# Kernel optimization log

Hardware: AMD Instinct MI355X
Metric: run time of the kernel (lower is better)

The kernel has to match this reference:

```python
import jax, jax.numpy as jnp
import numpy as np

B, N, M = 1, 16384, 16384
K_NEIGH = 16
KERNEL_SIZE = 15
C_IN, C_OUT = 64, 128
RADIUS = 1.0


def setup_inputs() -> dict:
    key = jax.random.key(0)
    k1, k2, k3, k4, k5 = jax.random.split(key, 5)
    query_points = jax.random.normal(k1, (B, N, 3), dtype=jnp.float32)
    support_points = query_points  # typical KPConv: support == query
    neighbor_idx = jax.random.randint(k2, (B, N, K_NEIGH), 0, M)
    features = jax.random.normal(k3, (B, M, C_IN), dtype=jnp.float32)
    weights = jax.random.normal(k4, (KERNEL_SIZE, C_IN, C_OUT), dtype=jnp.float32) * 0.005
    # kernel points: random unit directions scaled to radius, first fixed at center
    kp = jax.random.normal(k5, (KERNEL_SIZE, 3), dtype=jnp.float32)
    kp = kp / jnp.linalg.norm(kp, axis=1, keepdims=True) * RADIUS
    kernel_points = kp.at[0].set(jnp.zeros(3, dtype=jnp.float32))
    return {
        "query_points": query_points,
        "support_points": support_points,
        "neighbor_idx": neighbor_idx,
        "features": features,
        "weights": weights,
        "kernel_points": kernel_points,
    }


def reference(query_points, support_points, neighbor_idx, features, weights, kernel_points):
    # gather neighbor features and coords: (B,N,k,C), (B,N,k,3)
    gather = jax.vmap(lambda arr, idx: arr[idx])
    neighbor_feats = gather(features, neighbor_idx)
    neighbor_coords = gather(support_points, neighbor_idx)
    # relative coords to query: (B,N,k,3)
    rel = neighbor_coords - query_points[:, :, None, :]
    # distance to each kernel point: (B,N,k,P)
    diff = rel[:, :, :, None, :] - kernel_points[None, None, None, :, :]
    dists = jnp.linalg.norm(diff, axis=-1)
    # linear influence
    infl = jnp.clip(1.0 - dists / RADIUS, 0.0)
    # weighted sum over neighbors -> (B,N,P,C) without materializing (B,N,k,P,C)
    aggregated = jnp.einsum('bnkp,bnkc->bnpc', infl, neighbor_feats)
    # per-kernel-point matmul -> (B,N,C_out)
    return jnp.einsum('bnpc,pco->bno', aggregated, weights)
```

## Files before the change

kernel.cpp:

```cpp
#include <hip/hip_runtime.h>

typedef __attribute__((ext_vector_type(8))) short bf16x8;
typedef __attribute__((ext_vector_type(4))) float f32x4;

constexpr int N_PTS = 16384;
constexpr int KN = 16;
constexpr int P  = 15;
constexpr int CI = 64;
constexpr int CO = 128;
constexpr int QB = 16;
constexpr int KTOT   = P * CI;
constexpr int KSTEPS = KTOT / 32;
constexpr int NTILES = CO / 16;
constexpr int AGG_PITCH = KTOT + 8;

static __device__ __forceinline__ unsigned short f2bf(float f) {
    unsigned u = __float_as_uint(f);
    u = (u + 0x7fffu + ((u >> 16) & 1u)) >> 16;
    return (unsigned short)u;
}

__global__ __launch_bounds__(256) void prep_w(const float* __restrict__ W,
                                              unsigned short* __restrict__ WB) {
    const int t = blockIdx.x * 256 + threadIdx.x;
    const int s  = t >> 9;
    const int nt = (t >> 6) & 7;
    const int l  = t & 63;
    const int kb = s * 32 + ((l >> 4) * 8);
    const int o  = nt * 16 + (l & 15);
    unsigned short v[8];
    #pragma unroll
    for (int j = 0; j < 8; ++j) {
        v[j] = f2bf(W[(size_t)(kb + j) * CO + o]);
    }
    uint4 q;
    q.x = v[0] | ((unsigned)v[1] << 16);
    q.y = v[2] | ((unsigned)v[3] << 16);
    q.z = v[4] | ((unsigned)v[5] << 16);
    q.w = v[6] | ((unsigned)v[7] << 16);
    *(uint4*)&WB[(size_t)t * 8] = q;
}

__global__ __launch_bounds__(256) void kpconv_main(
    const float* __restrict__ query,
    const float* __restrict__ support,
    const int*   __restrict__ nidx,
    const float* __restrict__ feats,
    const unsigned short* __restrict__ WB,
    const float* __restrict__ kp,
    float* __restrict__ out)
{
    __shared__ float sKp[P][3];
    __shared__ int   sIdx[QB][KN];
    __shared__ __align__(16) float sInfl[QB][KN][16];
    __shared__ __align__(16) unsigned short sAgg[QB][AGG_PITCH];

    const int t  = threadIdx.x;
    const int n0 = blockIdx.x * QB;

    if (t < P * 3) ((float*)sKp)[t] = kp[t];
    __syncthreads();

    {
        const int pt = t >> 4, k = t & 15;
        const int n = n0 + pt;
        const int idx = nidx[n * KN + k];
        sIdx[pt][k] = idx;
        const float rx = support[idx * 3 + 0] - query[n * 3 + 0];
        const float ry = support[idx * 3 + 1] - query[n * 3 + 1];
        const float rz = support[idx * 3 + 2] - query[n * 3 + 2];
        #pragma unroll
        for (int p = 0; p < P; ++p) {
            const float dx = rx - sKp[p][0];
            const float dy = ry - sKp[p][1];
            const float dz = rz - sKp[p][2];
            sInfl[pt][k][p] = fmaxf(1.0f - sqrtf(dx*dx + dy*dy + dz*dz), 0.0f);
        }
        sInfl[pt][k][15] = 0.0f;
    }
    __syncthreads();

    {
        const int pt = t >> 4;
        const int c  = (t & 15) * 4;
        int idxv[KN];
        {
            const int4* ip = (const int4*)sIdx[pt];
            #pragma unroll
            for (int k4 = 0; k4 < 4; ++k4) {
                const int4 v = ip[k4];
                idxv[k4*4+0] = v.x; idxv[k4*4+1] = v.y;
                idxv[k4*4+2] = v.z; idxv[k4*4+3] = v.w;
            }
        }
        float acc[P][4];
        #pragma unroll
        for (int p = 0; p < P; ++p)
            #pragma unroll
            for (int j = 0; j < 4; ++j) acc[p][j] = 0.0f;

        #pragma unroll
        for (int k = 0; k < KN; ++k) {
            const float4 f = *(const float4*)&feats[(size_t)idxv[k] * CI + c];
            float iv[16];
            {
                const float4* ip = (const float4*)sInfl[pt][k];
                *(float4*)&iv[0]  = ip[0];
                *(float4*)&iv[4]  = ip[1];
                *(float4*)&iv[8]  = ip[2];
                *(float4*)&iv[12] = ip[3];
            }
            #pragma unroll
            for (int p = 0; p < P; ++p) {
                acc[p][0] = fmaf(iv[p], f.x, acc[p][0]);
                acc[p][1] = fmaf(iv[p], f.y, acc[p][1]);
                acc[p][2] = fmaf(iv[p], f.z, acc[p][2]);
                acc[p][3] = fmaf(iv[p], f.w, acc[p][3]);
            }
        }
        #pragma unroll
        for (int p = 0; p < P; ++p) {
            uint2 w;
            w.x = f2bf(acc[p][0]) | ((unsigned)f2bf(acc[p][1]) << 16);
            w.y = f2bf(acc[p][2]) | ((unsigned)f2bf(acc[p][3]) << 16);
            *(uint2*)&sAgg[pt][p * CI + c] = w;
        }
    }
    __syncthreads();

    {
        const int w = t >> 6, l = t & 63;
        const int row = l & 15;
        const int kq  = (l >> 4) * 8;
        f32x4 c0 = {0.f, 0.f, 0.f, 0.f};
        f32x4 c1 = {0.f, 0.f, 0.f, 0.f};
        const unsigned short* aggRow = &sAgg[row][kq];
        const unsigned short* wb0 = &WB[(size_t)((0 * NTILES + 2 * w) * 64 + l) * 8];
        #pragma unroll 2
        for (int s = 0; s < KSTEPS; ++s) {
            const bf16x8 a  = *(const bf16x8*)&aggRow[s * 32];
            const bf16x8 b0 = *(const bf16x8*)&wb0[(size_t)(s * NTILES) * 64 * 8];
            const bf16x8 b1 = *(const bf16x8*)&wb0[(size_t)(s * NTILES + 1) * 64 * 8];
            c0 = __builtin_amdgcn_mfma_f32_16x16x32_bf16(a, b0, c0, 0, 0, 0);
            c1 = __builtin_amdgcn_mfma_f32_16x16x32_bf16(a, b1, c1, 0, 0, 0);
        }
        const int rbase = (l >> 4) * 4;
        const int o0 = (2 * w) * 16 + (l & 15);
        #pragma unroll
        for (int r = 0; r < 4; ++r) {
            const int pt = rbase + r;
            out[(size_t)(n0 + pt) * CO + o0]      = c0[r];
            out[(size_t)(n0 + pt) * CO + o0 + 16] = c1[r];
        }
    }
}

extern "C" void kernel_launch(void* const* d_in, const int* in_sizes, int n_in,
                              void* d_out, int out_size, void* d_ws, size_t ws_size,
                              hipStream_t stream) {
    const float* query   = (const float*)d_in[0];
    const float* support = (const float*)d_in[1];
    const int*   nidx    = (const int*)d_in[2];
    const float* feats   = (const float*)d_in[3];
    const float* W       = (const float*)d_in[4];
    const float* kp      = (const float*)d_in[5];
    float* out = (float*)d_out;
    unsigned short* WB = (unsigned short*)d_ws;

    hipLaunchKernelGGL(prep_w, dim3(KSTEPS * NTILES * 64 / 256), dim3(256), 0, stream, W, WB);
    hipLaunchKernelGGL(kpconv_main, dim3(N_PTS / QB), dim3(256), 0, stream,
                       query, support, nidx, feats, WB, kp, out);
}
```

Baseline: 97.10 us.

## Split aggregation and GEMM into separate kernels with LDS-staged MFMA GEMM

```diff
diff --git a/kernel.cpp b/kernel.cpp
--- a/kernel.cpp
+++ b/kernel.cpp
@@ -12,7 +12,7 @@
 constexpr int KTOT   = P * CI;
 constexpr int KSTEPS = KTOT / 32;
 constexpr int NTILES = CO / 16;
-constexpr int AGG_PITCH = KTOT + 8;
+constexpr size_t AGG_BYTE_OFF = 262144;
 
 static __device__ __forceinline__ unsigned short f2bf(float f) {
     unsigned u = __float_as_uint(f);
@@ -20,40 +20,43 @@
     return (unsigned short)u;
 }
 
-__global__ __launch_bounds__(256) void prep_w(const float* __restrict__ W,
-                                              unsigned short* __restrict__ WB) {
-    const int t = blockIdx.x * 256 + threadIdx.x;
-    const int s  = t >> 9;
-    const int nt = (t >> 6) & 7;
-    const int l  = t & 63;
-    const int kb = s * 32 + ((l >> 4) * 8);
-    const int o  = nt * 16 + (l & 15);
-    unsigned short v[8];
-    #pragma unroll
-    for (int j = 0; j < 8; ++j) {
-        v[j] = f2bf(W[(size_t)(kb + j) * CO + o]);
-    }
-    uint4 q;
-    q.x = v[0] | ((unsigned)v[1] << 16);
-    q.y = v[2] | ((unsigned)v[3] << 16);
-    q.z = v[4] | ((unsigned)v[5] << 16);
-    q.w = v[6] | ((unsigned)v[7] << 16);
-    *(uint4*)&WB[(size_t)t * 8] = q;
-}
-
-__global__ __launch_bounds__(256) void kpconv_main(
+static __device__ __forceinline__ void gload16(const void* g, void* l) {
+    __builtin_amdgcn_global_load_lds(
+        (const __attribute__((address_space(1))) unsigned*)g,
+        (__attribute__((address_space(3))) unsigned*)l, 16, 0, 0);
+}
+
+__global__ __launch_bounds__(256) void kpconv_agg(
     const float* __restrict__ query,
     const float* __restrict__ support,
     const int*   __restrict__ nidx,
     const float* __restrict__ feats,
-    const unsigned short* __restrict__ WB,
+    const float* __restrict__ W,
     const float* __restrict__ kp,
-    float* __restrict__ out)
+    unsigned short* __restrict__ WB,
+    unsigned short* __restrict__ aggG)
 {
+    if (blockIdx.x < 60) {
+        const int t = blockIdx.x * 256 + threadIdx.x;
+        const int s  = t >> 9;
+        const int nt = (t >> 6) & 7;
+        const int l  = t & 63;
+        const int kb = s * 32 + ((l >> 4) * 8);
+        const int o  = nt * 16 + (l & 15);
+        unsigned short v[8];
+        #pragma unroll
+        for (int j = 0; j < 8; ++j) v[j] = f2bf(W[(size_t)(kb + j) * CO + o]);
+        uint4 q;
+        q.x = v[0] | ((unsigned)v[1] << 16);
+        q.y = v[2] | ((unsigned)v[3] << 16);
+        q.z = v[4] | ((unsigned)v[5] << 16);
+        q.w = v[6] | ((unsigned)v[7] << 16);
+        *(uint4*)&WB[(size_t)t * 8] = q;
+    }
+
     __shared__ float sKp[P][3];
     __shared__ int   sIdx[QB][KN];
     __shared__ __align__(16) float sInfl[QB][KN][16];
-    __shared__ __align__(16) unsigned short sAgg[QB][AGG_PITCH];
 
     const int t  = threadIdx.x;
     const int n0 = blockIdx.x * QB;
@@ -118,39 +121,72 @@
                 acc[p][3] = fmaf(iv[p], f.w, acc[p][3]);
             }
         }
+        const size_t rowBase = (size_t)(n0 + pt) * KTOT;
         #pragma unroll
         for (int p = 0; p < P; ++p) {
             uint2 w;
             w.x = f2bf(acc[p][0]) | ((unsigned)f2bf(acc[p][1]) << 16);
             w.y = f2bf(acc[p][2]) | ((unsigned)f2bf(acc[p][3]) << 16);
-            *(uint2*)&sAgg[pt][p * CI + c] = w;
-        }
-    }
-    __syncthreads();
-
-    {
-        const int w = t >> 6, l = t & 63;
-        const int row = l & 15;
-        const int kq  = (l >> 4) * 8;
-        f32x4 c0 = {0.f, 0.f, 0.f, 0.f};
-        f32x4 c1 = {0.f, 0.f, 0.f, 0.f};
-        const unsigned short* aggRow = &sAgg[row][kq];
-        const unsigned short* wb0 = &WB[(size_t)((0 * NTILES + 2 * w) * 64 + l) * 8];
-        #pragma unroll 2
-        for (int s = 0; s < KSTEPS; ++s) {
-            const bf16x8 a  = *(const bf16x8*)&aggRow[s * 32];
-            const bf16x8 b0 = *(const bf16x8*)&wb0[(size_t)(s * NTILES) * 64 * 8];
-            const bf16x8 b1 = *(const bf16x8*)&wb0[(size_t)(s * NTILES + 1) * 64 * 8];
-            c0 = __builtin_amdgcn_mfma_f32_16x16x32_bf16(a, b0, c0, 0, 0, 0);
-            c1 = __builtin_amdgcn_mfma_f32_16x16x32_bf16(a, b1, c1, 0, 0, 0);
-        }
-        const int rbase = (l >> 4) * 4;
-        const int o0 = (2 * w) * 16 + (l & 15);
-        #pragma unroll
-        for (int r = 0; r < 4; ++r) {
-            const int pt = rbase + r;
-            out[(size_t)(n0 + pt) * CO + o0]      = c0[r];
-            out[(size_t)(n0 + pt) * CO + o0 + 16] = c1[r];
+            *(uint2*)&aggG[rowBase + p * CI + c] = w;
+        }
+    }
+}
+
+__global__ __launch_bounds__(512) void kpconv_gemm(
+    const unsigned short* __restrict__ aggG,
+    const unsigned short* __restrict__ WB,
+    float* __restrict__ out)
+{
+    __shared__ __align__(16) unsigned short sA[2][4 * 64 * 8];
+    __shared__ __align__(16) unsigned short sB[2][8 * 64 * 8];
+
+    const int t = threadIdx.x;
+    const int w = t >> 6, l = t & 63;
+    const int n0 = blockIdx.x * 64;
+
+    const int rt = w & 3;
+    const int ng = w >> 2;
+    const int q  = l >> 4;
+
+    f32x4 acc[4] = {{0.f,0.f,0.f,0.f},{0.f,0.f,0.f,0.f},
+                    {0.f,0.f,0.f,0.f},{0.f,0.f,0.f,0.f}};
+
+    #define STAGE(s, b)                                                        \
+        do {                                                                   \
+            if (w < 4) {                                                       \
+                gload16(&aggG[(size_t)(n0 + l) * KTOT + (s) * 32 + w * 8],     \
+                        &sA[b][w * 512]);                                      \
+            } else {                                                           \
+                const int j = w - 4;                                           \
+                gload16(&WB[((size_t)(s) * 512 + j * 64 + l) * 8],             \
+                        &sB[b][j * 512]);                                      \
+                gload16(&WB[((size_t)(s) * 512 + (j + 4) * 64 + l) * 8],       \
+                        &sB[b][(j + 4) * 512]);                                \
+            }                                                                  \
+        } while (0)
+
+    STAGE(0, 0);
+    int b = 0;
+    for (int s = 0; s < KSTEPS; ++s) {
+        __syncthreads();
+        if (s + 1 < KSTEPS) STAGE(s + 1, b ^ 1);
+        const bf16x8 a = *(const bf16x8*)&sA[b][q * 512 + (rt * 16 + (l & 15)) * 8];
+        #pragma unroll
+        for (int nt = 0; nt < 4; ++nt) {
+            const bf16x8 bb = *(const bf16x8*)&sB[b][(ng * 4 + nt) * 512 + l * 8];
+            acc[nt] = __builtin_amdgcn_mfma_f32_16x16x32_bf16(a, bb, acc[nt], 0, 0, 0);
+        }
+        b ^= 1;
+    }
+    #undef STAGE
+
+    const int colBase = ng * 64;
+    const int rowBase = n0 + rt * 16 + (l >> 4) * 4;
+    #pragma unroll
+    for (int nt = 0; nt < 4; ++nt) {
+        #pragma unroll
+        for (int j = 0; j < 4; ++j) {
+            out[(size_t)(rowBase + j) * CO + colBase + nt * 16 + (l & 15)] = acc[nt][j];
         }
     }
 }
@@ -165,9 +201,12 @@
     const float* W       = (const float*)d_in[4];
     const float* kp      = (const float*)d_in[5];
     float* out = (float*)d_out;
-    unsigned short* WB = (unsigned short*)d_ws;
-
-    hipLaunchKernelGGL(prep_w, dim3(KSTEPS * NTILES * 64 / 256), dim3(256), 0, stream, W, WB);
-    hipLaunchKernelGGL(kpconv_main, dim3(N_PTS / QB), dim3(256), 0, stream,
-                       query, support, nidx, feats, WB, kp, out);
-}
+
+    unsigned short* WB   = (unsigned short*)d_ws;
+    unsigned short* aggG = (unsigned short*)((char*)d_ws + AGG_BYTE_OFF);
+
+    hipLaunchKernelGGL(kpconv_agg, dim3(N_PTS / QB), dim3(256), 0, stream,
+                       query, support, nidx, feats, W, kp, WB, aggG);
+    hipLaunchKernelGGL(kpconv_gemm, dim3(N_PTS / 64), dim3(512), 0, stream,
+                       aggG, WB, out);
+}
```

Result: slower. 105.2 us (+8.4%).

## Compute neighbor aggregation with MFMA and permute weights to match layout

Applied to the files above, without the earlier changes.

```diff
diff --git a/kernel.cpp b/kernel.cpp
--- a/kernel.cpp
+++ b/kernel.cpp
@@ -9,15 +9,21 @@
 constexpr int CI = 64;
 constexpr int CO = 128;
 constexpr int QB = 16;
-constexpr int KTOT   = P * CI;
-constexpr int KSTEPS = KTOT / 32;
-constexpr int NTILES = CO / 16;
-constexpr int AGG_PITCH = KTOT + 8;
+constexpr int KP = 1024;
+constexpr int KSTEPS = KP / 32;
+constexpr int IPITCH = 32;
+constexpr int APITCH = KP + 8;
 
 static __device__ __forceinline__ unsigned short f2bf(float f) {
     unsigned u = __float_as_uint(f);
     u = (u + 0x7fffu + ((u >> 16) & 1u)) >> 16;
     return (unsigned short)u;
+}
+
+static __device__ __forceinline__ unsigned cvt_pk_bf16(float lo, float hi) {
+    unsigned r;
+    asm("v_cvt_pk_bf16_f32 %0, %1, %2" : "=v"(r) : "v"(lo), "v"(hi));
+    return r;
 }
 
 __global__ __launch_bounds__(256) void prep_w(const float* __restrict__ W,
@@ -26,22 +32,28 @@
     const int s  = t >> 9;
     const int nt = (t >> 6) & 7;
     const int l  = t & 63;
-    const int kb = s * 32 + ((l >> 4) * 8);
+    const int q  = l >> 4;
     const int o  = nt * 16 + (l & 15);
     unsigned short v[8];
     #pragma unroll
     for (int j = 0; j < 8; ++j) {
-        v[j] = f2bf(W[(size_t)(kb + j) * CO + o]);
+        const int kp_ = s * 32 + q * 8 + j;
+        const int prodlane = kp_ >> 4;
+        const int ct = (kp_ >> 2) & 3;
+        const int jr = kp_ & 3;
+        const int p  = (prodlane >> 4) * 4 + jr;
+        const int c  = (prodlane & 15) + ct * 16;
+        v[j] = (p < P) ? f2bf(W[(size_t)(p * CI + c) * CO + o]) : (unsigned short)0;
     }
-    uint4 q;
-    q.x = v[0] | ((unsigned)v[1] << 16);
-    q.y = v[2] | ((unsigned)v[3] << 16);
-    q.z = v[4] | ((unsigned)v[5] << 16);
-    q.w = v[6] | ((unsigned)v[7] << 16);
-    *(uint4*)&WB[(size_t)t * 8] = q;
+    uint4 qv;
+    qv.x = v[0] | ((unsigned)v[1] << 16);
+    qv.y = v[2] | ((unsigned)v[3] << 16);
+    qv.z = v[4] | ((unsigned)v[5] << 16);
+    qv.w = v[6] | ((unsigned)v[7] << 16);
+    *(uint4*)&WB[(size_t)t * 8] = qv;
 }
 
-__global__ __launch_bounds__(256) void kpconv_main(
+__global__ __launch_bounds__(256) void kpconv_fused(
     const float* __restrict__ query,
     const float* __restrict__ support,
     const int*   __restrict__ nidx,
@@ -52,13 +64,20 @@
 {
     __shared__ float sKp[P][3];
     __shared__ int   sIdx[QB][KN];
-    __shared__ __align__(16) float sInfl[QB][KN][16];
-    __shared__ __align__(16) unsigned short sAgg[QB][AGG_PITCH];
+    __shared__ __align__(16) unsigned short sInflT[QB * 16 * IPITCH];
+    __shared__ __align__(16) unsigned short sAgg[QB * APITCH];
 
     const int t  = threadIdx.x;
     const int n0 = blockIdx.x * QB;
+    const int l  = t & 63, w = t >> 6, q = l >> 4;
 
     if (t < P * 3) ((float*)sKp)[t] = kp[t];
+
+    {
+        const uint4 z = {0u, 0u, 0u, 0u};
+        uint4* dst = (uint4*)sInflT;
+        dst[t] = z; dst[t + 256] = z; dst[t + 512] = z; dst[t + 768] = z;
+    }
     __syncthreads();
 
     {
@@ -69,83 +88,73 @@
         const float rx = support[idx * 3 + 0] - query[n * 3 + 0];
         const float ry = support[idx * 3 + 1] - query[n * 3 + 1];
         const float rz = support[idx * 3 + 2] - query[n * 3 + 2];
+        unsigned short* row0 = &sInflT[(pt * 16) * IPITCH + k];
         #pragma unroll
         for (int p = 0; p < P; ++p) {
             const float dx = rx - sKp[p][0];
             const float dy = ry - sKp[p][1];
             const float dz = rz - sKp[p][2];
-            sInfl[pt][k][p] = fmaxf(1.0f - sqrtf(dx*dx + dy*dy + dz*dz), 0.0f);
-        }
-        sInfl[pt][k][15] = 0.0f;
-    }
-    __syncthreads();
-
-    {
-        const int pt = t >> 4;
-        const int c  = (t & 15) * 4;
-        int idxv[KN];
-        {
-            const int4* ip = (const int4*)sIdx[pt];
-            #pragma unroll
-            for (int k4 = 0; k4 < 4; ++k4) {
-                const int4 v = ip[k4];
-                idxv[k4*4+0] = v.x; idxv[k4*4+1] = v.y;
-                idxv[k4*4+2] = v.z; idxv[k4*4+3] = v.w;
-            }
-        }
-        float acc[P][4];
-        #pragma unroll
-        for (int p = 0; p < P; ++p)
-            #pragma unroll
-            for (int j = 0; j < 4; ++j) acc[p][j] = 0.0f;
-
-        #pragma unroll
-        for (int k = 0; k < KN; ++k) {
-            const float4 f = *(const float4*)&feats[(size_t)idxv[k] * CI + c];
-            float iv[16];
-            {
-                const float4* ip = (const float4*)sInfl[pt][k];
-                *(float4*)&iv[0]  = ip[0];
-                *(float4*)&iv[4]  = ip[1];
-                *(float4*)&iv[8]  = ip[2];
-                *(float4*)&iv[12] = ip[3];
-            }
-            #pragma unroll
-            for (int p = 0; p < P; ++p) {
-                acc[p][0] = fmaf(iv[p], f.x, acc[p][0]);
-                acc[p][1] = fmaf(iv[p], f.y, acc[p][1]);
-                acc[p][2] = fmaf(iv[p], f.z, acc[p][2]);
-                acc[p][3] = fmaf(iv[p], f.w, acc[p][3]);
-            }
-        }
-        #pragma unroll
-        for (int p = 0; p < P; ++p) {
-            uint2 w;
-            w.x = f2bf(acc[p][0]) | ((unsigned)f2bf(acc[p][1]) << 16);
-            w.y = f2bf(acc[p][2]) | ((unsigned)f2bf(acc[p][3]) << 16);
-            *(uint2*)&sAgg[pt][p * CI + c] = w;
+            const float infl = fmaxf(1.0f - sqrtf(dx*dx + dy*dy + dz*dz), 0.0f);
+            row0[p * IPITCH] = f2bf(infl);
         }
     }
     __syncthreads();
 
     {
-        const int w = t >> 6, l = t & 63;
-        const int row = l & 15;
-        const int kq  = (l >> 4) * 8;
+        const f32x4 zero4 = {0.f, 0.f, 0.f, 0.f};
+        for (int i = 0; i < 4; ++i) {
+            const int pt = w * 4 + i;
+            const bf16x8 a = *(const bf16x8*)&sInflT[(pt * 16 + (l & 15)) * IPITCH + q * 8];
+            float fv[4][8];
+            #pragma unroll
+            for (int j = 0; j < 8; ++j) {
+                const int idx = sIdx[pt][(q & 1) * 8 + j];
+                const float* rowp = feats + (size_t)idx * CI + (l & 15);
+                #pragma unroll
+                for (int ct = 0; ct < 4; ++ct) fv[ct][j] = rowp[ct * 16];
+            }
+            f32x4 aggv[4];
+            #pragma unroll
+            for (int ct = 0; ct < 4; ++ct) {
+                unsigned b0 = cvt_pk_bf16(fv[ct][0], fv[ct][1]);
+                unsigned b1 = cvt_pk_bf16(fv[ct][2], fv[ct][3]);
+                unsigned b2 = cvt_pk_bf16(fv[ct][4], fv[ct][5]);
+                unsigned b3 = cvt_pk_bf16(fv[ct][6], fv[ct][7]);
+                if (l >= 32) { b0 = 0; b1 = 0; b2 = 0; b3 = 0; }
+                union { unsigned u[4]; bf16x8 v; } bu;
+                bu.u[0] = b0; bu.u[1] = b1; bu.u[2] = b2; bu.u[3] = b3;
+                aggv[ct] = __builtin_amdgcn_mfma_f32_16x16x32_bf16(a, bu.v, zero4, 0, 0, 0);
+            }
+            uint4 w0, w1;
+            w0.x = cvt_pk_bf16(aggv[0][0], aggv[0][1]);
+            w0.y = cvt_pk_bf16(aggv[0][2], aggv[0][3]);
+            w0.z = cvt_pk_bf16(aggv[1][0], aggv[1][1]);
+            w0.w = cvt_pk_bf16(aggv[1][2], aggv[1][3]);
+            w1.x = cvt_pk_bf16(aggv[2][0], aggv[2][1]);
+            w1.y = cvt_pk_bf16(aggv[2][2], aggv[2][3]);
+            w1.z = cvt_pk_bf16(aggv[3][0], aggv[3][1]);
+            w1.w = cvt_pk_bf16(aggv[3][2], aggv[3][3]);
+            uint4* dst = (uint4*)&sAgg[pt * APITCH + l * 16];
+            dst[0] = w0; dst[1] = w1;
+        }
+    }
+    __syncthreads();
+
+    {
         f32x4 c0 = {0.f, 0.f, 0.f, 0.f};
         f32x4 c1 = {0.f, 0.f, 0.f, 0.f};
-        const unsigned short* aggRow = &sAgg[row][kq];
-        const unsigned short* wb0 = &WB[(size_t)((0 * NTILES + 2 * w) * 64 + l) * 8];
+        const unsigned short* aggRow = &sAgg[(l & 15) * APITCH + q * 8];
+        const unsigned short* wb0 = &WB[(size_t)(2 * w * 64 + l) * 8];
         #pragma unroll 2
         for (int s = 0; s < KSTEPS; ++s) {
             const bf16x8 a  = *(const bf16x8*)&aggRow[s * 32];
-            const bf16x8 b0 = *(const bf16x8*)&wb0[(size_t)(s * NTILES) * 64 * 8];
-            const bf16x8 b1 = *(const bf16x8*)&wb0[(size_t)(s * NTILES + 1) * 64 * 8];
+            const bf16x8 b0 = *(const bf16x8*)&wb0[(size_t)s * 4096];
+            const bf16x8 b1 = *(const bf16x8*)&wb0[(size_t)s * 4096 + 512];
             c0 = __builtin_amdgcn_mfma_f32_16x16x32_bf16(a, b0, c0, 0, 0, 0);
             c1 = __builtin_amdgcn_mfma_f32_16x16x32_bf16(a, b1, c1, 0, 0, 0);
         }
-        const int rbase = (l >> 4) * 4;
-        const int o0 = (2 * w) * 16 + (l & 15);
+        const int rbase = q * 4;
+        const int o0 = 2 * w * 16 + (l & 15);
         #pragma unroll
         for (int r = 0; r < 4; ++r) {
             const int pt = rbase + r;
@@ -167,7 +176,7 @@
     float* out = (float*)d_out;
     unsigned short* WB = (unsigned short*)d_ws;
 
-    hipLaunchKernelGGL(prep_w, dim3(KSTEPS * NTILES * 64 / 256), dim3(256), 0, stream, W, WB);
-    hipLaunchKernelGGL(kpconv_main, dim3(N_PTS / QB), dim3(256), 0, stream,
+    hipLaunchKernelGGL(prep_w, dim3(KSTEPS * 8 * 64 / 256), dim3(256), 0, stream, W, WB);
+    hipLaunchKernelGGL(kpconv_fused, dim3(N_PTS / QB), dim3(256), 0, stream,
                        query, support, nidx, feats, WB, kp, out);
 }
```

New measurement: 96.89 us. No clear change (-0.2%).

## Split aggregation and GEMM into separate kernels with larger GEMM tiles

Applied to the files above, without the earlier changes.

```diff
diff --git a/kernel.cpp b/kernel.cpp
--- a/kernel.cpp
+++ b/kernel.cpp
@@ -11,8 +11,7 @@
 constexpr int QB = 16;
 constexpr int KTOT   = P * CI;
 constexpr int KSTEPS = KTOT / 32;
-constexpr int NTILES = CO / 16;
-constexpr int AGG_PITCH = KTOT + 8;
+constexpr size_t AGG_OFF = 262144;
 
 static __device__ __forceinline__ unsigned short f2bf(float f) {
     unsigned u = __float_as_uint(f);
@@ -20,19 +19,21 @@
     return (unsigned short)u;
 }
 
+static __device__ __forceinline__ void gload16(const void* g, void* l) {
+    __builtin_amdgcn_global_load_lds(
+        (const __attribute__((address_space(1))) unsigned*)g,
+        (__attribute__((address_space(3))) unsigned*)l, 16, 0, 0);
+}
+
 __global__ __launch_bounds__(256) void prep_w(const float* __restrict__ W,
                                               unsigned short* __restrict__ WB) {
     const int t = blockIdx.x * 256 + threadIdx.x;
-    const int s  = t >> 9;
-    const int nt = (t >> 6) & 7;
     const int l  = t & 63;
-    const int kb = s * 32 + ((l >> 4) * 8);
-    const int o  = nt * 16 + (l & 15);
+    const int k0 = (t >> 9) * 32 + ((l >> 4) * 8);
+    const int o  = ((t >> 6) & 7) * 16 + (l & 15);
     unsigned short v[8];
     #pragma unroll
-    for (int j = 0; j < 8; ++j) {
-        v[j] = f2bf(W[(size_t)(kb + j) * CO + o]);
-    }
+    for (int j = 0; j < 8; ++j) v[j] = f2bf(W[(size_t)(k0 + j) * CO + o]);
     uint4 q;
     q.x = v[0] | ((unsigned)v[1] << 16);
     q.y = v[2] | ((unsigned)v[3] << 16);
@@ -41,19 +42,17 @@
     *(uint4*)&WB[(size_t)t * 8] = q;
 }
 
-__global__ __launch_bounds__(256) void kpconv_main(
+__global__ __launch_bounds__(256) void kpconv_agg(
     const float* __restrict__ query,
     const float* __restrict__ support,
     const int*   __restrict__ nidx,
     const float* __restrict__ feats,
-    const unsigned short* __restrict__ WB,
     const float* __restrict__ kp,
-    float* __restrict__ out)
+    unsigned short* __restrict__ aggG)
 {
     __shared__ float sKp[P][3];
     __shared__ int   sIdx[QB][KN];
     __shared__ __align__(16) float sInfl[QB][KN][16];
-    __shared__ __align__(16) unsigned short sAgg[QB][AGG_PITCH];
 
     const int t  = threadIdx.x;
     const int n0 = blockIdx.x * QB;
@@ -118,40 +117,65 @@
                 acc[p][3] = fmaf(iv[p], f.w, acc[p][3]);
             }
         }
+        const size_t rowBase = (size_t)(n0 + pt) * KTOT;
         #pragma unroll
         for (int p = 0; p < P; ++p) {
             uint2 w;
             w.x = f2bf(acc[p][0]) | ((unsigned)f2bf(acc[p][1]) << 16);
             w.y = f2bf(acc[p][2]) | ((unsigned)f2bf(acc[p][3]) << 16);
-            *(uint2*)&sAgg[pt][p * CI + c] = w;
-        }
+            *(uint2*)&aggG[rowBase + p * CI + c] = w;
+        }
+    }
+}
+
+__global__ __launch_bounds__(512) void kpconv_gemm(
+    const unsigned short* __restrict__ aggG,
+    const unsigned short* __restrict__ WB,
+    float* __restrict__ out)
+{
+    __shared__ __align__(16) unsigned short sA[KSTEPS * 4 * 64 * 8];
+
+    const int t = threadIdx.x;
+    const int w = t >> 6, l = t & 63;
+    const int n0 = blockIdx.x * 64;
+
+    #pragma unroll
+    for (int i = 0; i < 15; ++i) {
+        const int chunk = i * 512 + t;
+        const int g  = chunk >> 6;
+        const int cl = chunk & 63;
+        const int s  = g >> 2, rt = g & 3;
+        const unsigned short* src =
+            aggG + (size_t)(n0 + rt * 16 + (cl & 15)) * KTOT + s * 32 + ((cl >> 4) * 8);
+        gload16(src, &sA[(size_t)chunk * 8]);
     }
     __syncthreads();
 
-    {
-        const int w = t >> 6, l = t & 63;
-        const int row = l & 15;
-        const int kq  = (l >> 4) * 8;
-        f32x4 c0 = {0.f, 0.f, 0.f, 0.f};
-        f32x4 c1 = {0.f, 0.f, 0.f, 0.f};
-        const unsigned short* aggRow = &sAgg[row][kq];
-        const unsigned short* wb0 = &WB[(size_t)((0 * NTILES + 2 * w) * 64 + l) * 8];
-        #pragma unroll 2
-        for (int s = 0; s < KSTEPS; ++s) {
-            const bf16x8 a  = *(const bf16x8*)&aggRow[s * 32];
-            const bf16x8 b0 = *(const bf16x8*)&wb0[(size_t)(s * NTILES) * 64 * 8];
-            const bf16x8 b1 = *(const bf16x8*)&wb0[(size_t)(s * NTILES + 1) * 64 * 8];
-            c0 = __builtin_amdgcn_mfma_f32_16x16x32_bf16(a, b0, c0, 0, 0, 0);
-            c1 = __builtin_amdgcn_mfma_f32_16x16x32_bf16(a, b1, c1, 0, 0, 0);
-        }
-        const int rbase = (l >> 4) * 4;
-        const int o0 = (2 * w) * 16 + (l & 15);
-        #pragma unroll
-        for (int r = 0; r < 4; ++r) {
-            const int pt = rbase + r;
-            out[(size_t)(n0 + pt) * CO + o0]      = c0[r];
-            out[(size_t)(n0 + pt) * CO + o0 + 16] = c1[r];
-        }
+    const int rh = (w & 1) * 2;
+    const int nh = (w >> 1) * 2;
+    f32x4 acc00 = {0.f,0.f,0.f,0.f}, acc01 = {0.f,0.f,0.f,0.f};
+    f32x4 acc10 = {0.f,0.f,0.f,0.f}, acc11 = {0.f,0.f,0.f,0.f};
+
+    #pragma unroll 3
+    for (int s = 0; s < KSTEPS; ++s) {
+        const bf16x8 a0 = *(const bf16x8*)&sA[((s * 4 + rh    ) * 64 + l) * 8];
+        const bf16x8 a1 = *(const bf16x8*)&sA[((s * 4 + rh + 1) * 64 + l) * 8];
+        const bf16x8 b0 = *(const bf16x8*)&WB[((size_t)(s * 8 + nh    ) * 64 + l) * 8];
+        const bf16x8 b1 = *(const bf16x8*)&WB[((size_t)(s * 8 + nh + 1) * 64 + l) * 8];
+        acc00 = __builtin_amdgcn_mfma_f32_16x16x32_bf16(a0, b0, acc00, 0, 0, 0);
+        acc01 = __builtin_amdgcn_mfma_f32_16x16x32_bf16(a0, b1, acc01, 0, 0, 0);
+        acc10 = __builtin_amdgcn_mfma_f32_16x16x32_bf16(a1, b0, acc10, 0, 0, 0);
+        acc11 = __builtin_amdgcn_mfma_f32_16x16x32_bf16(a1, b1, acc11, 0, 0, 0);
+    }
+
+    const int col0 = (w >> 1) * 32 + (l & 15);
+    const int row0 = n0 + (w & 1) * 32 + (l >> 4) * 4;
+    #pragma unroll
+    for (int r = 0; r < 4; ++r) {
+        out[(size_t)(row0 + r) * CO + col0]           = acc00[r];
+        out[(size_t)(row0 + r) * CO + col0 + 16]      = acc01[r];
+        out[(size_t)(row0 + 16 + r) * CO + col0]      = acc10[r];
+        out[(size_t)(row0 + 16 + r) * CO + col0 + 16] = acc11[r];
     }
 }
 
@@ -165,9 +189,13 @@
     const float* W       = (const float*)d_in[4];
     const float* kp      = (const float*)d_in[5];
     float* out = (float*)d_out;
-    unsigned short* WB = (unsigned short*)d_ws;
-
-    hipLaunchKernelGGL(prep_w, dim3(KSTEPS * NTILES * 64 / 256), dim3(256), 0, stream, W, WB);
-    hipLaunchKernelGGL(kpconv_main, dim3(N_PTS / QB), dim3(256), 0, stream,
-                       query, support, nidx, feats, WB, kp, out);
-}
+
+    unsigned short* WB   = (unsigned short*)d_ws;
+    unsigned short* aggG = (unsigned short*)((char*)d_ws + AGG_OFF);
+
+    hipLaunchKernelGGL(prep_w, dim3(60), dim3(256), 0, stream, W, WB);
+    hipLaunchKernelGGL(kpconv_agg, dim3(N_PTS / QB), dim3(256), 0, stream,
+                       query, support, nidx, feats, kp, aggG);
+    hipLaunchKernelGGL(kpconv_gemm, dim3(N_PTS / 64), dim3(512), 0, stream,
+                       aggG, WB, out);
+}
```

Result: slower. 102.8 us (+5.8%).
